# Optimization experiments

Measured on AMD Instinct MI355X. Metric: run time of the kernel, lower is better.

The kernel has to match this reference:

```python
import jax, jax.numpy as jnp
import numpy as np

D, M, L = 4096, 1024, 8192


def _prelu(x, a):
    # torch.nn.functional.prelu with scalar weight a (shape [1])
    return jnp.where(x >= 0, x, a * x)


def setup_inputs() -> dict:
    key = jax.random.key(0)
    ks = jax.random.split(key, 13)
    f32 = jnp.float32
    return {
        "input": jax.random.normal(ks[0], (1, L), f32),
        "query": jax.random.normal(ks[1], (1, L), f32),
        "F_i": jax.random.normal(ks[2], (D, L), f32),
        "F_q": jax.random.normal(ks[3], (D, L), f32),
        "keys": jax.random.normal(ks[4], (D, M), f32),
        "memory_nodes": jax.random.normal(ks[5], (D, M), f32),
        "U": jax.random.normal(ks[6], (D, D), f32),
        "V": jax.random.normal(ks[7], (D, D), f32),
        "W": jax.random.normal(ks[8], (D, D), f32),
        "R": jax.random.normal(ks[9], (D, D), f32),
        "H": jax.random.normal(ks[10], (D, D), f32),
        "a_mem": jax.random.normal(ks[11], (1,), f32),
        "a_out": jax.random.normal(ks[12], (1,), f32),
    }


def reference(input, query, F_i, F_q, keys, memory_nodes, U, V, W, R, H, a_mem, a_out):
    # input_step: s = sum_i F[:, i] * input[0, i]  ==  F @ input[0], shape [D, 1]
    s_in = (F_i @ input[0])[:, None]
    s_q = (F_q @ query[0])[:, None]

    # memory_step
    # g = sigmoid(s_in^T @ memory + s_in^T @ keys)  -> [1, M]
    g = jax.nn.sigmoid(s_in.T @ memory_nodes + s_in.T @ keys)
    # candidate memory is computed (with PReLU) but never used in the original forward
    cand = _prelu(U @ memory_nodes + V @ keys + W @ s_in, a_mem)  # noqa: F841 (dead, as in source)
    # per-column gated scale of old memory, then L2-normalize columns (dim=0, eps=1e-12)
    mem = memory_nodes * (1.0 + g)  # broadcast [D,M]*[1,M]
    mem = mem / jnp.maximum(jnp.linalg.norm(mem, axis=0, keepdims=True), 1e-12)

    # output_step
    p = jax.nn.softmax(s_q.T @ mem, axis=1)        # [1, M]
    u = mem @ p[0][:, None]                        # [D, 1] == sum_i p_i * mem[:, i]
    y = R @ _prelu(s_q + H @ u, a_out)             # [D, 1]
    return y
```

## Files before the change

kernel.cpp:

```cpp
#include <hip/hip_runtime.h>

#define DD 4096
#define MM 1024
#define LL 8192

template <int NCOLS, bool PRELU>
__global__ __launch_bounds__(256) void gemv_wpr(const float* __restrict__ A,
                                                const float* __restrict__ x,
                                                const float* __restrict__ bias,
                                                const float* __restrict__ slope,
                                                float* __restrict__ y) {
    const int wave = threadIdx.x >> 6;
    const int lane = threadIdx.x & 63;
    const int row = (blockIdx.x << 2) + wave;
    const float4* __restrict__ Arow =
        reinterpret_cast<const float4*>(A + (size_t)row * NCOLS);
    const float4* __restrict__ x4 = reinterpret_cast<const float4*>(x);
    float ax = 0.f, ay = 0.f, az = 0.f, aw = 0.f;
#pragma unroll 8
    for (int k = lane; k < NCOLS / 4; k += 64) {
        float4 a = Arow[k];
        float4 b = x4[k];
        ax = fmaf(a.x, b.x, ax);
        ay = fmaf(a.y, b.y, ay);
        az = fmaf(a.z, b.z, az);
        aw = fmaf(a.w, b.w, aw);
    }
    float acc = (ax + ay) + (az + aw);
#pragma unroll
    for (int off = 32; off; off >>= 1) acc += __shfl_down(acc, off, 64);
    if (lane == 0) {
        if constexpr (PRELU) {
            float t = bias[row] + acc;
            y[row] = (t >= 0.f) ? t : slope[0] * t;
        } else {
            y[row] = acc;
        }
    }
}

__global__ __launch_bounds__(256) void col_accum(const float* __restrict__ mem,
                                                 const float* __restrict__ sq,
                                                 float* __restrict__ zacc,
                                                 float* __restrict__ sqacc) {
    const int ROWS = 64;
    const int m = blockIdx.x * 256 + threadIdx.x;
    const int r0 = blockIdx.y * ROWS;
    float z = 0.f, s = 0.f;
#pragma unroll 4
    for (int r = 0; r < ROWS; ++r) {
        float w = sq[r0 + r];
        float v = mem[(size_t)(r0 + r) * MM + m];
        z = fmaf(w, v, z);
        s = fmaf(v, v, s);
    }
    atomicAdd(&zacc[m], z);
    atomicAdd(&sqacc[m], s);
}

__global__ __launch_bounds__(1024) void softmax_fold(const float* __restrict__ zacc,
                                                     const float* __restrict__ sqacc,
                                                     float* __restrict__ qout) {
    __shared__ float sh[16];
    __shared__ float red[2];
    const int m = threadIdx.x;
    const int wave = m >> 6, lane = m & 63;
    const float rn = rsqrtf(fmaxf(sqacc[m], 1e-24f));
    const float t = zacc[m] * rn;
    float mx = t;
#pragma unroll
    for (int off = 32; off; off >>= 1) mx = fmaxf(mx, __shfl_down(mx, off, 64));
    if (lane == 0) sh[wave] = mx;
    __syncthreads();
    if (m == 0) {
        float v = sh[0];
        for (int i = 1; i < 16; ++i) v = fmaxf(v, sh[i]);
        red[0] = v;
    }
    __syncthreads();
    const float e = __expf(t - red[0]);
    float s = e;
#pragma unroll
    for (int off = 32; off; off >>= 1) s += __shfl_down(s, off, 64);
    if (lane == 0) sh[wave] = s;
    __syncthreads();
    if (m == 0) {
        float v = 0.f;
        for (int i = 0; i < 16; ++i) v += sh[i];
        red[1] = v;
    }
    __syncthreads();
    qout[m] = (e / red[1]) * rn;
}

extern "C" void kernel_launch(void* const* d_in, const int* in_sizes, int n_in,
                              void* d_out, int out_size, void* d_ws, size_t ws_size,
                              hipStream_t stream) {
    const float* query = (const float*)d_in[1];
    const float* F_q   = (const float*)d_in[3];
    const float* mem   = (const float*)d_in[5];
    const float* R     = (const float*)d_in[9];
    const float* H     = (const float*)d_in[10];
    const float* a_out = (const float*)d_in[12];
    float* out = (float*)d_out;

    float* ws    = (float*)d_ws;
    float* s_q   = ws;
    float* zacc  = ws + 4096;
    float* sqacc = ws + 5120;
    float* qv    = ws + 6144;
    float* u     = ws + 7168;
    float* v     = ws + 11264;

    gemv_wpr<LL, false><<<DD / 4, 256, 0, stream>>>(F_q, query, nullptr, nullptr, s_q);

    hipMemsetAsync(zacc, 0, 2048 * sizeof(float), stream);

    dim3 gcol(MM / 256, DD / 64);
    col_accum<<<gcol, 256, 0, stream>>>(mem, s_q, zacc, sqacc);

    softmax_fold<<<1, 1024, 0, stream>>>(zacc, sqacc, qv);

    gemv_wpr<MM, false><<<DD / 4, 256, 0, stream>>>(mem, qv, nullptr, nullptr, u);

    gemv_wpr<DD, true><<<DD / 4, 256, 0, stream>>>(H, u, s_q, a_out, v);

    gemv_wpr<DD, false><<<DD / 4, 256, 0, stream>>>(R, v, nullptr, nullptr, out);
}
```

Before: 469.9 us.

## Fuse all GEMV stages into one persistent kernel with grid barriers

Replaces the six separate launches (four GEMVs, column accumulation, softmax) with a single persistent kernel of 512 blocks that moves between stages through a software grid barrier built on atomics. The aim is to remove per-launch overhead and the drain and refill gaps between kernels. The column accumulation pass now reads float4 per thread over 16 rows per block. The design depends on all 512 blocks being resident at once, which is not guaranteed, so the barrier could deadlock. Each stage also has fewer blocks than before, and the softmax runs on a single block while the others wait.

```diff
diff --git a/kernel.cpp b/kernel.cpp
--- a/kernel.cpp
+++ b/kernel.cpp
@@ -3,22 +3,34 @@
 #define DD 4096
 #define MM 1024
 #define LL 8192
+#define NBLK 512
 
-template <int NCOLS, bool PRELU>
-__global__ __launch_bounds__(256) void gemv_wpr(const float* __restrict__ A,
-                                                const float* __restrict__ x,
-                                                const float* __restrict__ bias,
-                                                const float* __restrict__ slope,
-                                                float* __restrict__ y) {
-    const int wave = threadIdx.x >> 6;
-    const int lane = threadIdx.x & 63;
-    const int row = (blockIdx.x << 2) + wave;
-    const float4* __restrict__ Arow =
-        reinterpret_cast<const float4*>(A + (size_t)row * NCOLS);
-    const float4* __restrict__ x4 = reinterpret_cast<const float4*>(x);
+__device__ __forceinline__ void grid_barrier(unsigned* cnt, unsigned* gen) {
+    __syncthreads();
+    __threadfence();
+    if (threadIdx.x == 0) {
+        unsigned g = __hip_atomic_load(gen, __ATOMIC_RELAXED, __HIP_MEMORY_SCOPE_AGENT);
+        unsigned a = __hip_atomic_fetch_add(cnt, 1u, __ATOMIC_ACQ_REL, __HIP_MEMORY_SCOPE_AGENT);
+        if (a == NBLK - 1) {
+            __hip_atomic_store(cnt, 0u, __ATOMIC_RELAXED, __HIP_MEMORY_SCOPE_AGENT);
+            __hip_atomic_fetch_add(gen, 1u, __ATOMIC_ACQ_REL, __HIP_MEMORY_SCOPE_AGENT);
+        } else {
+            while (__hip_atomic_load(gen, __ATOMIC_ACQUIRE, __HIP_MEMORY_SCOPE_AGENT) == g) {
+                __builtin_amdgcn_s_sleep(8);
+            }
+        }
+    }
+    __syncthreads();
+    __threadfence();
+}
+
+template <int N4>
+__device__ __forceinline__ float wave_row_dot(const float4* __restrict__ Arow,
+                                              const float4* __restrict__ x4,
+                                              int lane) {
     float ax = 0.f, ay = 0.f, az = 0.f, aw = 0.f;
 #pragma unroll 8
-    for (int k = lane; k < NCOLS / 4; k += 64) {
+    for (int k = lane; k < N4; k += 64) {
         float4 a = Arow[k];
         float4 b = x4[k];
         ax = fmaf(a.x, b.x, ax);
@@ -29,68 +41,129 @@
     float acc = (ax + ay) + (az + aw);
 #pragma unroll
     for (int off = 32; off; off >>= 1) acc += __shfl_down(acc, off, 64);
-    if (lane == 0) {
-        if constexpr (PRELU) {
-            float t = bias[row] + acc;
-            y[row] = (t >= 0.f) ? t : slope[0] * t;
-        } else {
-            y[row] = acc;
+    return acc;
+}
+
+__global__ __launch_bounds__(256, 2) void entnet_fused(
+    const float* __restrict__ F_q, const float* __restrict__ query,
+    const float* __restrict__ mem, const float* __restrict__ H,
+    const float* __restrict__ R, const float* __restrict__ a_out,
+    float* __restrict__ out, float* __restrict__ ws) {
+    float* s_q = ws;
+    float* zacc = ws + 4096;
+    float* sqacc = ws + 5120;
+    unsigned* bar = (unsigned*)(ws + 6144);
+    float* qv = ws + 6656;
+    float* u = ws + 7680;
+    float* v = ws + 11776;
+
+    const int b = blockIdx.x, tid = threadIdx.x;
+    const int wave = tid >> 6, lane = tid & 63;
+    __shared__ float sh3[4];
+    __shared__ float red3[2];
+
+    {
+        const float4* x4 = reinterpret_cast<const float4*>(query);
+#pragma unroll
+        for (int i = 0; i < 2; ++i) {
+            const int row = b * 8 + wave * 2 + i;
+            float acc = wave_row_dot<LL / 4>(
+                reinterpret_cast<const float4*>(F_q + (size_t)row * LL), x4, lane);
+            if (lane == 0) s_q[row] = acc;
         }
     }
-}
+    grid_barrier(bar, bar + 1);
 
-__global__ __launch_bounds__(256) void col_accum(const float* __restrict__ mem,
-                                                 const float* __restrict__ sq,
-                                                 float* __restrict__ zacc,
-                                                 float* __restrict__ sqacc) {
-    const int ROWS = 64;
-    const int m = blockIdx.x * 256 + threadIdx.x;
-    const int r0 = blockIdx.y * ROWS;
-    float z = 0.f, s = 0.f;
+    if (b < 256) {
+        const int r0 = b * 16;
+        const float4* m4p = reinterpret_cast<const float4*>(mem);
+        float z0 = 0.f, z1 = 0.f, z2 = 0.f, z3 = 0.f;
+        float s0 = 0.f, s1 = 0.f, s2 = 0.f, s3 = 0.f;
 #pragma unroll 4
-    for (int r = 0; r < ROWS; ++r) {
-        float w = sq[r0 + r];
-        float v = mem[(size_t)(r0 + r) * MM + m];
-        z = fmaf(w, v, z);
-        s = fmaf(v, v, s);
+        for (int r = 0; r < 16; ++r) {
+            const float w = s_q[r0 + r];
+            const float4 m4 = m4p[(size_t)(r0 + r) * (MM / 4) + tid];
+            z0 = fmaf(w, m4.x, z0); s0 = fmaf(m4.x, m4.x, s0);
+            z1 = fmaf(w, m4.y, z1); s1 = fmaf(m4.y, m4.y, s1);
+            z2 = fmaf(w, m4.z, z2); s2 = fmaf(m4.z, m4.z, s2);
+            z3 = fmaf(w, m4.w, z3); s3 = fmaf(m4.w, m4.w, s3);
+        }
+        atomicAdd(&zacc[4 * tid + 0], z0); atomicAdd(&zacc[4 * tid + 1], z1);
+        atomicAdd(&zacc[4 * tid + 2], z2); atomicAdd(&zacc[4 * tid + 3], z3);
+        atomicAdd(&sqacc[4 * tid + 0], s0); atomicAdd(&sqacc[4 * tid + 1], s1);
+        atomicAdd(&sqacc[4 * tid + 2], s2); atomicAdd(&sqacc[4 * tid + 3], s3);
     }
-    atomicAdd(&zacc[m], z);
-    atomicAdd(&sqacc[m], s);
-}
+    grid_barrier(bar, bar + 1);
 
-__global__ __launch_bounds__(1024) void softmax_fold(const float* __restrict__ zacc,
-                                                     const float* __restrict__ sqacc,
-                                                     float* __restrict__ qout) {
-    __shared__ float sh[16];
-    __shared__ float red[2];
-    const int m = threadIdx.x;
-    const int wave = m >> 6, lane = m & 63;
-    const float rn = rsqrtf(fmaxf(sqacc[m], 1e-24f));
-    const float t = zacc[m] * rn;
-    float mx = t;
+    if (b == 0) {
+        float t[4], rn[4], e[4];
+        float mx = -1e30f;
 #pragma unroll
-    for (int off = 32; off; off >>= 1) mx = fmaxf(mx, __shfl_down(mx, off, 64));
-    if (lane == 0) sh[wave] = mx;
-    __syncthreads();
-    if (m == 0) {
-        float v = sh[0];
-        for (int i = 1; i < 16; ++i) v = fmaxf(v, sh[i]);
-        red[0] = v;
+        for (int j = 0; j < 4; ++j) {
+            const int m = tid + 256 * j;
+            rn[j] = rsqrtf(fmaxf(sqacc[m], 1e-24f));
+            t[j] = zacc[m] * rn[j];
+            mx = fmaxf(mx, t[j]);
+        }
+#pragma unroll
+        for (int off = 32; off; off >>= 1) mx = fmaxf(mx, __shfl_down(mx, off, 64));
+        if (lane == 0) sh3[wave] = mx;
+        __syncthreads();
+        if (tid == 0) red3[0] = fmaxf(fmaxf(sh3[0], sh3[1]), fmaxf(sh3[2], sh3[3]));
+        __syncthreads();
+        float ssum = 0.f;
+#pragma unroll
+        for (int j = 0; j < 4; ++j) { e[j] = __expf(t[j] - red3[0]); ssum += e[j]; }
+#pragma unroll
+        for (int off = 32; off; off >>= 1) ssum += __shfl_down(ssum, off, 64);
+        if (lane == 0) sh3[wave] = ssum;
+        __syncthreads();
+        if (tid == 0) red3[1] = sh3[0] + sh3[1] + sh3[2] + sh3[3];
+        __syncthreads();
+        const float inv = 1.f / red3[1];
+#pragma unroll
+        for (int j = 0; j < 4; ++j) qv[tid + 256 * j] = e[j] * rn[j] * inv;
     }
-    __syncthreads();
-    const float e = __expf(t - red[0]);
-    float s = e;
+    grid_barrier(bar, bar + 1);
+
+    {
+        const float4* x4 = reinterpret_cast<const float4*>(qv);
 #pragma unroll
-    for (int off = 32; off; off >>= 1) s += __shfl_down(s, off, 64);
-    if (lane == 0) sh[wave] = s;
-    __syncthreads();
-    if (m == 0) {
-        float v = 0.f;
-        for (int i = 0; i < 16; ++i) v += sh[i];
-        red[1] = v;
+        for (int i = 0; i < 2; ++i) {
+            const int row = b * 8 + wave * 2 + i;
+            float acc = wave_row_dot<MM / 4>(
+                reinterpret_cast<const float4*>(mem + (size_t)row * MM), x4, lane);
+            if (lane == 0) u[row] = acc;
+        }
     }
-    __syncthreads();
-    qout[m] = (e / red[1]) * rn;
+    grid_barrier(bar, bar + 1);
+
+    {
+        const float4* x4 = reinterpret_cast<const float4*>(u);
+        const float slope = a_out[0];
+#pragma unroll
+        for (int i = 0; i < 2; ++i) {
+            const int row = b * 8 + wave * 2 + i;
+            float acc = wave_row_dot<DD / 4>(
+                reinterpret_cast<const float4*>(H + (size_t)row * DD), x4, lane);
+            if (lane == 0) {
+                float t = s_q[row] + acc;
+                v[row] = (t >= 0.f) ? t : slope * t;
+            }
+        }
+    }
+    grid_barrier(bar, bar + 1);
+
+    {
+        const float4* x4 = reinterpret_cast<const float4*>(v);
+#pragma unroll
+        for (int i = 0; i < 2; ++i) {
+            const int row = b * 8 + wave * 2 + i;
+            float acc = wave_row_dot<DD / 4>(
+                reinterpret_cast<const float4*>(R + (size_t)row * DD), x4, lane);
+            if (lane == 0) out[row] = acc;
+        }
+    }
 }
 
 extern "C" void kernel_launch(void* const* d_in, const int* in_sizes, int n_in,
@@ -103,27 +176,9 @@
     const float* H     = (const float*)d_in[10];
     const float* a_out = (const float*)d_in[12];
     float* out = (float*)d_out;
+    float* ws  = (float*)d_ws;
 
-    float* ws    = (float*)d_ws;
-    float* s_q   = ws;
-    float* zacc  = ws + 4096;
-    float* sqacc = ws + 5120;
-    float* qv    = ws + 6144;
-    float* u     = ws + 7168;
-    float* v     = ws + 11264;
+    hipMemsetAsync(ws + 4096, 0, 2050 * sizeof(float), stream);
 
-    gemv_wpr<LL, false><<<DD / 4, 256, 0, stream>>>(F_q, query, nullptr, nullptr, s_q);
-
-    hipMemsetAsync(zacc, 0, 2048 * sizeof(float), stream);
-
-    dim3 gcol(MM / 256, DD / 64);
-    col_accum<<<gcol, 256, 0, stream>>>(mem, s_q, zacc, sqacc);
-
-    softmax_fold<<<1, 1024, 0, stream>>>(zacc, sqacc, qv);
-
-    gemv_wpr<MM, false><<<DD / 4, 256, 0, stream>>>(mem, qv, nullptr, nullptr, u);
-
-    gemv_wpr<DD, true><<<DD / 4, 256, 0, stream>>>(H, u, s_q, a_out, v);
-
-    gemv_wpr<DD, false><<<DD / 4, 256, 0, stream>>>(R, v, nullptr, nullptr, out);
+    entnet_fused<<<NBLK, 256, 0, stream>>>(F_q, query, mem, H, R, a_out, out, ws);
 }
```

After: 1.137 ms. 2.42x slower.
